# Kernel tuning notes

Measured on AMD Instinct MI355X. Metric: run time of the kernel, lower is better.

## Reference

```python
import jax, jax.numpy as jnp
import numpy as np

B, S, D, H = 4, 4096, 1024, 16
DV = D // H


def setup_inputs() -> dict:
    key = jax.random.key(0)
    ks = jax.random.split(key, 8)
    def gl(k, shape):  # glorot-uniform-ish init
        fan_in, fan_out = shape[0], shape[-1]
        lim = np.sqrt(6.0 / (fan_in + fan_out)).astype(np.float32)
        return jax.random.uniform(k, shape, jnp.float32, -lim, lim)
    return {
        "q": jax.random.normal(ks[0], (B, S, D), jnp.float32),
        "k": jax.random.normal(ks[1], (B, S, D), jnp.float32),
        "v": jax.random.normal(ks[2], (B, S, D), jnp.float32),
        "wq": gl(ks[3], (D, H)), "bq": jnp.zeros((H,), jnp.float32),
        "wk": gl(ks[4], (D, H)), "bk": jnp.zeros((H,), jnp.float32),
        "wv": gl(ks[5], (D, D)), "bv": jnp.zeros((D,), jnp.float32),
        "wo": gl(ks[6], (D, D)), "bo": jnp.zeros((D,), jnp.float32),
    }


def reference(q, k, v, wq, bq, wk, bk, wv, bv, wo, bo):
    b, s, d = q.shape
    h = wq.shape[1]
    dv = d // h
    # per-head scalar queries/keys, sigmoid feature map phi
    qh = jax.nn.sigmoid(q @ wq + bq)                 # (B,S,H)
    kh = jax.nn.sigmoid(k @ wk + bk)                 # (B,S,H)
    vh = (v @ wv + bv).reshape(b, s, h, dv)          # (B,S,H,DV)
    # phi(k)^T @ v contracts seq -> per-head summary (B,H,DV)
    kv = jnp.einsum("bsh,bshd->bhd", kh, vh)
    # NOTE: original tf code cumsums over axis=1 of (B,H,1,DV): the HEAD axis
    state = jnp.cumsum(kv, axis=1)                   # (B,H,DV)
    # phi(q) @ state, broadcast over seq
    out_h = jnp.einsum("bsh,bhd->bshd", qh, state)   # (B,S,H,DV)
    concat = out_h.reshape(b, s, d)
    return concat @ wo + bo                          # (B,S,D)
```

## Files before the change

kernel.cpp:

```cpp
#include <hip/hip_runtime.h>

#define SS 4096
#define DD 1024
#define HH 16

typedef float nfloat4 __attribute__((ext_vector_type(4)));
typedef __attribute__((ext_vector_type(8))) short bf16x8;
typedef __attribute__((ext_vector_type(4))) float f32x4;

__device__ __forceinline__ short f2bf(float f) {
  union { float f; unsigned u; } z; z.f = f;
  return (short)((z.u + 0x8000u) >> 16);
}

__global__ __launch_bounds__(256) void k_wfrag(
    const float* __restrict__ wq, const float* __restrict__ wk,
    short* __restrict__ wf)
{
  const int m = blockIdx.x;
  const float* __restrict__ w = m ? wk : wq;
  short* __restrict__ dst = wf + m * 16384;
  for (int p = threadIdx.x; p < 2048; p += 256) {
    const int t = p >> 6, l = p & 63;
    const int kbase = t*32 + ((l >> 4) * 8), col = l & 15;
    short v[8];
#pragma unroll
    for (int e = 0; e < 8; ++e)
      v[e] = f2bf(w[(size_t)(kbase + e)*HH + col]);
    short* o = dst + (size_t)p * 8;
#pragma unroll
    for (int e = 0; e < 8; ++e) o[e] = v[e];
  }
}

__global__ __launch_bounds__(256, 4) void k_kh(
    const float* __restrict__ k, const short* __restrict__ wf,
    const float* __restrict__ bk, float* __restrict__ kh,
    float* __restrict__ ksp)
{
  const int t = threadIdx.x;
  const int wid = t >> 6, lane = t & 63;
  const int s0 = blockIdx.x * 16;
  const short* __restrict__ wfm = wf + 16384;

  __shared__ short xs[16 * 1024];
  __shared__ float red[1024];

  float4 f[16];
  {
    const float* srow = k + (size_t)s0 * DD + t*4;
#pragma unroll
    for (int j = 0; j < 16; ++j)
      f[j] = *(const float4*)(srow + (size_t)j * DD);
  }
  const short* __restrict__ wfw = wfm + (size_t)(wid*8*64 + lane) * 8;
  bf16x8 afrag[8];
#pragma unroll
  for (int tt = 0; tt < 8; ++tt)
    afrag[tt] = *(const bf16x8*)(wfw + (size_t)(tt*64) * 8);
  __builtin_amdgcn_sched_barrier(0);

#pragma unroll
  for (int j = 0; j < 16; ++j) {
    short4 b4;
    b4.x = f2bf(f[j].x); b4.y = f2bf(f[j].y);
    b4.z = f2bf(f[j].z); b4.w = f2bf(f[j].w);
    const int colb = (t*8) ^ ((j & 7) << 4);
    *(short4*)((char*)xs + j*2048 + colb) = b4;
  }
  __syncthreads();

  const int row = lane & 15, g = lane >> 4;
  const char* __restrict__ xrow = (const char*)xs + row*2048;
  f32x4 acc = {0.f, 0.f, 0.f, 0.f};
#pragma unroll
  for (int tt = 0; tt < 8; ++tt) {
    const int colb = ((wid*256 + tt*32 + g*8) * 2) ^ ((row & 7) << 4);
    const bf16x8 bb = *(const bf16x8*)(xrow + colb);
    acc = __builtin_amdgcn_mfma_f32_16x16x32_bf16(afrag[tt], bb, acc, 0, 0, 0);
  }
  *(f32x4*)&red[(wid*64 + lane)*4] = acc;
  __syncthreads();
  const int orow = t >> 4, ohead = t & 15;
  const int lane2 = ((ohead >> 2) << 4) + orow;
  const int j = ohead & 3;
  const float sacc = red[0*256 + lane2*4 + j] + red[1*256 + lane2*4 + j]
                   + red[2*256 + lane2*4 + j] + red[3*256 + lane2*4 + j];
  const float sig = 1.f/(1.f + __expf(-(sacc + bk[ohead])));
  kh[(size_t)(s0 + orow)*HH + ohead] = sig;
  __syncthreads();
  red[t] = sig;
  __syncthreads();
  if (t < 16) {
    float s = 0.f;
#pragma unroll
    for (int r = 0; r < 16; ++r) s += red[r*16 + t];
    ksp[blockIdx.x*16 + t] = s;
  }
}

__global__ __launch_bounds__(256, 8) void k_kvt(
    const float* __restrict__ v, const float* __restrict__ kh,
    float* __restrict__ part)
{
  const int schunk = blockIdx.x;
  const int dchunk = blockIdx.y;
  const int b = blockIdx.z;
  const int t = threadIdx.x;
  const int c = t & 31;
  const int hh2 = (t >> 5) & 1;
  const int g = t >> 6;
  const int d0 = dchunk*128 + c*4;
  float acc[8][4];
#pragma unroll
  for (int h = 0; h < 8; ++h) {
    acc[h][0] = 0.f; acc[h][1] = 0.f; acc[h][2] = 0.f; acc[h][3] = 0.f;
  }
#pragma unroll 2
  for (int jj = 0; jj < 32; ++jj) {
    const int s = (jj*4 + g)*32 + schunk;
    const size_t rb = (size_t)(b*SS + s);
    const float4 v4 = *(const float4*)(v + rb*DD + d0);
    const float4* khp = (const float4*)(kh + rb*HH) + hh2*2;
    const float4 k0 = khp[0], k1 = khp[1];
    const float kk[8] = {k0.x,k0.y,k0.z,k0.w, k1.x,k1.y,k1.z,k1.w};
#pragma unroll
    for (int h = 0; h < 8; ++h) {
      acc[h][0] = fmaf(kk[h], v4.x, acc[h][0]);
      acc[h][1] = fmaf(kk[h], v4.y, acc[h][1]);
      acc[h][2] = fmaf(kk[h], v4.z, acc[h][2]);
      acc[h][3] = fmaf(kk[h], v4.w, acc[h][3]);
    }
  }
  __shared__ float lds[4][2][128];
  const size_t pbase = (size_t)((b*8 + dchunk)*32 + schunk) * 2048;
#pragma unroll
  for (int h = 0; h < 8; ++h) {
    *(float4*)&lds[g][hh2][c*4] =
        make_float4(acc[h][0], acc[h][1], acc[h][2], acc[h][3]);
    __syncthreads();
    {
      const int hh2r = t >> 7, dl = t & 127;
      const float sum = lds[0][hh2r][dl] + lds[1][hh2r][dl]
                      + lds[2][hh2r][dl] + lds[3][hh2r][dl];
      part[pbase + (hh2r*8 + h)*128 + dl] = sum;
    }
    __syncthreads();
  }
}

__global__ __launch_bounds__(256, 8) void k_red(
    const float* __restrict__ part, float* __restrict__ kvt)
{
  const int dchunk = blockIdx.x;
  const int b = blockIdx.y;
  const int hq = blockIdx.z;
  const int t = threadIdx.x;
  const size_t pb = (size_t)((b*8 + dchunk)*32) * 2048;
#pragma unroll
  for (int ho = 0; ho < 2; ++ho) {
    const int h = hq*4 + ho*2 + (t >> 7), dl = t & 127;
    float s = 0.f;
#pragma unroll 8
    for (int sc = 0; sc < 32; ++sc)
      s += part[pb + (size_t)sc*2048 + h*128 + dl];
    kvt[(size_t)(b*16 + h)*1024 + dchunk*128 + dl] = s;
  }
}

__global__ __launch_bounds__(256, 4) void k_kv(
    const float* __restrict__ kvt, const float* __restrict__ wv,
    float* __restrict__ kvp)
{
  const int h = blockIdx.x;
  const int b = blockIdx.y;
  const int dq = blockIdx.z;
  const int t = threadIdx.x;
  const int w = t >> 6, lane = t & 63;
  __shared__ float kvs[256];
  __shared__ float red[256];
  kvs[t] = kvt[(size_t)(b*16 + h)*1024 + dq*256 + t];
  __syncthreads();
  const float* __restrict__ wp = wv + (size_t)(dq*256 + w*64)*DD + h*64 + lane;
  float acc = 0.f;
#pragma unroll 16
  for (int i = 0; i < 64; ++i)
    acc = fmaf(kvs[w*64 + i], wp[(size_t)i*DD], acc);
  red[t] = acc;
  __syncthreads();
  if (t < 64)
    kvp[((size_t)(b*16 + h)*4 + dq)*64 + t] =
        red[t] + red[64+t] + red[128+t] + red[192+t];
}

__global__ __launch_bounds__(256) void k_kvfin(
    const float* __restrict__ kvp, const float* __restrict__ ksp,
    const float* __restrict__ bv, float* __restrict__ kv)
{
  const int b = blockIdx.x;
  const int t = threadIdx.x;
  __shared__ float red[256];
  __shared__ float ksum[16];
  float s = 0.f;
#pragma unroll
  for (int m = 0; m < 16; ++m)
    s += ksp[b*4096 + m*256 + t];
  red[t] = s;
  __syncthreads();
  if (t < 16) {
    float ks = 0.f;
#pragma unroll
    for (int g = 0; g < 16; ++g) ks += red[g*16 + t];
    ksum[t] = ks;
  }
  __syncthreads();
#pragma unroll
  for (int j = 0; j < 4; ++j) {
    const int idx = j*256 + t;
    const int h = idx >> 6;
    const float* kp = kvp + (size_t)(b*16 + h)*256 + (idx & 63);
    kv[(size_t)b*1024 + idx] =
        kp[0] + kp[64] + kp[128] + kp[192] + ksum[h]*bv[idx];
  }
}

__global__ __launch_bounds__(256) void k_w2(
    const float* __restrict__ kv, const float* __restrict__ wo,
    float* __restrict__ W2)
{
  const int bh = blockIdx.x;
  const int b = bh >> 4, h = bh & 15;
  const int t = threadIdx.x;
  __shared__ float st[64];
  if (t < 64) {
    float s = 0.f;
    for (int hp = 0; hp <= h; ++hp) s += kv[(size_t)b*1024 + hp*64 + t];
    st[t] = s;
  }
  __syncthreads();
  const int d0 = t * 4;
  float4 acc = {0.f, 0.f, 0.f, 0.f};
#pragma unroll 4
  for (int dv = 0; dv < 64; ++dv) {
    const float sv = st[dv];
    const float4 w4 = *(const float4*)(wo + (size_t)(h*64 + dv)*DD + d0);
    acc.x = fmaf(sv, w4.x, acc.x);
    acc.y = fmaf(sv, w4.y, acc.y);
    acc.z = fmaf(sv, w4.z, acc.z);
    acc.w = fmaf(sv, w4.w, acc.w);
  }
  *(float4*)(W2 + (size_t)(b*HH + h)*DD + d0) = acc;
}

__global__ __launch_bounds__(256, 4) void k_qout(
    const float* __restrict__ q, const short* __restrict__ wf,
    const float* __restrict__ bq, const float* __restrict__ W2,
    const float* __restrict__ bo, float* __restrict__ out)
{
  const int t = threadIdx.x;
  const int wid = t >> 6, lane = t & 63;
  const int tile = blockIdx.x;
  const int b = tile >> 8;
  const int s0 = tile * 16;

  __shared__ short xs[16 * 1024];
  __shared__ float red[1024];
  __shared__ float qs[256];

  float4 f[16];
  {
    const float* srow = q + (size_t)s0 * DD + t*4;
#pragma unroll
    for (int j = 0; j < 16; ++j)
      f[j] = *(const float4*)(srow + (size_t)j * DD);
  }
  const short* __restrict__ wfw = wf + (size_t)(wid*8*64 + lane) * 8;
  bf16x8 afrag[8];
#pragma unroll
  for (int tt = 0; tt < 8; ++tt)
    afrag[tt] = *(const bf16x8*)(wfw + (size_t)(tt*64) * 8);
  __builtin_amdgcn_sched_barrier(0);

#pragma unroll
  for (int j = 0; j < 16; ++j) {
    short4 b4;
    b4.x = f2bf(f[j].x); b4.y = f2bf(f[j].y);
    b4.z = f2bf(f[j].z); b4.w = f2bf(f[j].w);
    const int colb = (t*8) ^ ((j & 7) << 4);
    *(short4*)((char*)xs + j*2048 + colb) = b4;
  }
  __syncthreads();

  const int row = lane & 15, g = lane >> 4;
  const char* __restrict__ xrow = (const char*)xs + row*2048;
  f32x4 acc = {0.f, 0.f, 0.f, 0.f};
#pragma unroll
  for (int tt = 0; tt < 8; ++tt) {
    const int colb = ((wid*256 + tt*32 + g*8) * 2) ^ ((row & 7) << 4);
    const bf16x8 bb = *(const bf16x8*)(xrow + colb);
    acc = __builtin_amdgcn_mfma_f32_16x16x32_bf16(afrag[tt], bb, acc, 0, 0, 0);
  }
  *(f32x4*)&red[(wid*64 + lane)*4] = acc;
  __syncthreads();
  {
    const int orow = t >> 4, ohead = t & 15;
    const int lane2 = ((ohead >> 2) << 4) + orow;
    const int j = ohead & 3;
    const float sacc = red[0*256 + lane2*4 + j] + red[1*256 + lane2*4 + j]
                     + red[2*256 + lane2*4 + j] + red[3*256 + lane2*4 + j];
    const float val = sacc + bq[ohead];
    qs[orow*16 + ohead] = 1.f/(1.f + __expf(-val));
  }
  __syncthreads();

  float4 w2[16];
  {
    const float* w2p = W2 + (size_t)(b*HH)*DD + t*4;
#pragma unroll
    for (int h = 0; h < 16; ++h) w2[h] = *(const float4*)(w2p + h*DD);
  }
  const float4 bo4 = *(const float4*)(bo + t*4);

#pragma unroll
  for (int r = 0; r < 16; ++r) {
    float4 o = bo4;
#pragma unroll
    for (int h = 0; h < 16; ++h) {
      const float qv = qs[r*16 + h];
      o.x = fmaf(qv, w2[h].x, o.x);
      o.y = fmaf(qv, w2[h].y, o.y);
      o.z = fmaf(qv, w2[h].z, o.z);
      o.w = fmaf(qv, w2[h].w, o.w);
    }
    nfloat4 ov = { o.x, o.y, o.z, o.w };
    nfloat4* dst = (nfloat4*)(out + (size_t)(s0 + r)*DD + t*4);
    __builtin_nontemporal_store(ov, dst);
  }
}

extern "C" void kernel_launch(void* const* d_in, const int* in_sizes, int n_in,
                              void* d_out, int out_size, void* d_ws, size_t ws_size,
                              hipStream_t stream)
{
  const float* q  = (const float*)d_in[0];
  const float* k  = (const float*)d_in[1];
  const float* v  = (const float*)d_in[2];
  const float* wq = (const float*)d_in[3];
  const float* bq = (const float*)d_in[4];
  const float* wk = (const float*)d_in[5];
  const float* bk = (const float*)d_in[6];
  const float* wv = (const float*)d_in[7];
  const float* bv = (const float*)d_in[8];
  const float* wo = (const float*)d_in[9];
  const float* bo = (const float*)d_in[10];
  float* out = (float*)d_out;
  float* ws  = (float*)d_ws;

  float* kh  = ws;
  float* kvt = ws + 262144;
  float* kvp = ws + 327680;
  float* ksp = ws + 344064;
  float* kv  = ws + 360448;
  float* W2  = ws + 364544;
  short* wf  = (short*)(ws + 430080);
  float* part = out;

  hipLaunchKernelGGL(k_wfrag, dim3(2), dim3(256), 0, stream,
                     wq, wk, wf);
  hipLaunchKernelGGL(k_kh, dim3(1024), dim3(256), 0, stream,
                     k, wf, bk, kh, ksp);
  hipLaunchKernelGGL(k_kvt, dim3(32, 8, 4), dim3(256), 0, stream,
                     v, kh, part);
  hipLaunchKernelGGL(k_red, dim3(8, 4, 4), dim3(256), 0, stream,
                     part, kvt);
  hipLaunchKernelGGL(k_kv, dim3(16, 4, 4), dim3(256), 0, stream,
                     kvt, wv, kvp);
  hipLaunchKernelGGL(k_kvfin, dim3(4), dim3(256), 0, stream,
                     kvp, ksp, bv, kv);
  hipLaunchKernelGGL(k_w2, dim3(64), dim3(256), 0, stream,
                     kv, wo, W2);
  hipLaunchKernelGGL(k_qout, dim3(1024), dim3(256), 0, stream,
                     q, wf, bq, W2, bo, out);
}
```

Measured before the change: 79.13 us.

## Process two row tiles per block in k_kh and k_qout with prefetch of next tile

Each block of k_kh and k_qout now handles two 16-row tiles instead of one, halving the grid. The weight fragments and W2/bias loads are amortized over both tiles, and the second tile's input rows are loaded into registers while the first tile is converted and multiplied. The aim is to hide global load latency and cut per-block setup. The cost is more registers per thread (launch bounds lowered to 2 blocks per SM) and fewer blocks to spread across CUs.

```diff
diff --git a/kernel.cpp b/kernel.cpp
--- a/kernel.cpp
+++ b/kernel.cpp
@@ -33,69 +33,83 @@
   }
 }
 
-__global__ __launch_bounds__(256, 4) void k_kh(
+__global__ __launch_bounds__(256, 2) void k_kh(
     const float* __restrict__ k, const short* __restrict__ wf,
     const float* __restrict__ bk, float* __restrict__ kh,
     float* __restrict__ ksp)
 {
   const int t = threadIdx.x;
   const int wid = t >> 6, lane = t & 63;
-  const int s0 = blockIdx.x * 16;
+  const int tb = blockIdx.x * 2;
   const short* __restrict__ wfm = wf + 16384;
 
   __shared__ short xs[16 * 1024];
   __shared__ float red[1024];
 
+  const short* __restrict__ wfw = wfm + (size_t)(wid*8*64 + lane) * 8;
+  bf16x8 afrag[8];
+#pragma unroll
+  for (int tt = 0; tt < 8; ++tt)
+    afrag[tt] = *(const bf16x8*)(wfw + (size_t)(tt*64) * 8);
+
   float4 f[16];
   {
-    const float* srow = k + (size_t)s0 * DD + t*4;
+    const float* srow = k + (size_t)(tb*16) * DD + t*4;
 #pragma unroll
     for (int j = 0; j < 16; ++j)
       f[j] = *(const float4*)(srow + (size_t)j * DD);
   }
-  const short* __restrict__ wfw = wfm + (size_t)(wid*8*64 + lane) * 8;
-  bf16x8 afrag[8];
-#pragma unroll
-  for (int tt = 0; tt < 8; ++tt)
-    afrag[tt] = *(const bf16x8*)(wfw + (size_t)(tt*64) * 8);
   __builtin_amdgcn_sched_barrier(0);
 
-#pragma unroll
-  for (int j = 0; j < 16; ++j) {
-    short4 b4;
-    b4.x = f2bf(f[j].x); b4.y = f2bf(f[j].y);
-    b4.z = f2bf(f[j].z); b4.w = f2bf(f[j].w);
-    const int colb = (t*8) ^ ((j & 7) << 4);
-    *(short4*)((char*)xs + j*2048 + colb) = b4;
-  }
-  __syncthreads();
-
   const int row = lane & 15, g = lane >> 4;
-  const char* __restrict__ xrow = (const char*)xs + row*2048;
-  f32x4 acc = {0.f, 0.f, 0.f, 0.f};
-#pragma unroll
-  for (int tt = 0; tt < 8; ++tt) {
-    const int colb = ((wid*256 + tt*32 + g*8) * 2) ^ ((row & 7) << 4);
-    const bf16x8 bb = *(const bf16x8*)(xrow + colb);
-    acc = __builtin_amdgcn_mfma_f32_16x16x32_bf16(afrag[tt], bb, acc, 0, 0, 0);
-  }
-  *(f32x4*)&red[(wid*64 + lane)*4] = acc;
-  __syncthreads();
   const int orow = t >> 4, ohead = t & 15;
   const int lane2 = ((ohead >> 2) << 4) + orow;
-  const int j = ohead & 3;
-  const float sacc = red[0*256 + lane2*4 + j] + red[1*256 + lane2*4 + j]
-                   + red[2*256 + lane2*4 + j] + red[3*256 + lane2*4 + j];
-  const float sig = 1.f/(1.f + __expf(-(sacc + bk[ohead])));
-  kh[(size_t)(s0 + orow)*HH + ohead] = sig;
-  __syncthreads();
-  red[t] = sig;
-  __syncthreads();
-  if (t < 16) {
-    float s = 0.f;
-#pragma unroll
-    for (int r = 0; r < 16; ++r) s += red[r*16 + t];
-    ksp[blockIdx.x*16 + t] = s;
+  const int jr = ohead & 3;
+  const float biasv = bk[ohead];
+
+#pragma unroll
+  for (int i = 0; i < 2; ++i) {
+    const int s0 = (tb + i) * 16;
+#pragma unroll
+    for (int j = 0; j < 16; ++j) {
+      short4 b4;
+      b4.x = f2bf(f[j].x); b4.y = f2bf(f[j].y);
+      b4.z = f2bf(f[j].z); b4.w = f2bf(f[j].w);
+      const int colb = (t*8) ^ ((j & 7) << 4);
+      *(short4*)((char*)xs + j*2048 + colb) = b4;
+    }
+    if (i == 0) {
+      const float* srow = k + (size_t)((tb + 1)*16) * DD + t*4;
+#pragma unroll
+      for (int j = 0; j < 16; ++j)
+        f[j] = *(const float4*)(srow + (size_t)j * DD);
+      __builtin_amdgcn_sched_barrier(0);
+    }
+    __syncthreads();
+
+    const char* __restrict__ xrow = (const char*)xs + row*2048;
+    f32x4 acc = {0.f, 0.f, 0.f, 0.f};
+#pragma unroll
+    for (int tt = 0; tt < 8; ++tt) {
+      const int colb = ((wid*256 + tt*32 + g*8) * 2) ^ ((row & 7) << 4);
+      const bf16x8 bb = *(const bf16x8*)(xrow + colb);
+      acc = __builtin_amdgcn_mfma_f32_16x16x32_bf16(afrag[tt], bb, acc, 0, 0, 0);
+    }
+    *(f32x4*)&red[(wid*64 + lane)*4] = acc;
+    __syncthreads();
+    const float sacc = red[0*256 + lane2*4 + jr] + red[1*256 + lane2*4 + jr]
+                     + red[2*256 + lane2*4 + jr] + red[3*256 + lane2*4 + jr];
+    const float sig = 1.f/(1.f + __expf(-(sacc + biasv)));
+    kh[(size_t)(s0 + orow)*HH + ohead] = sig;
+    __syncthreads();
+    red[t] = sig;
+    __syncthreads();
+    if (t < 16) {
+      float s = 0.f;
+#pragma unroll
+      for (int r = 0; r < 16; ++r) s += red[r*16 + t];
+      ksp[(tb + i)*16 + t] = s;
+    }
   }
 }
 
@@ -252,67 +266,24 @@
   *(float4*)(W2 + (size_t)(b*HH + h)*DD + d0) = acc;
 }
 
-__global__ __launch_bounds__(256, 4) void k_qout(
+__global__ __launch_bounds__(256, 2) void k_qout(
     const float* __restrict__ q, const short* __restrict__ wf,
     const float* __restrict__ bq, const float* __restrict__ W2,
     const float* __restrict__ bo, float* __restrict__ out)
 {
   const int t = threadIdx.x;
   const int wid = t >> 6, lane = t & 63;
-  const int tile = blockIdx.x;
-  const int b = tile >> 8;
-  const int s0 = tile * 16;
-
+  const int tb = blockIdx.x * 2;
+  const int b = tb >> 8;
   __shared__ short xs[16 * 1024];
   __shared__ float red[1024];
   __shared__ float qs[256];
 
-  float4 f[16];
-  {
-    const float* srow = q + (size_t)s0 * DD + t*4;
-#pragma unroll
-    for (int j = 0; j < 16; ++j)
-      f[j] = *(const float4*)(srow + (size_t)j * DD);
-  }
   const short* __restrict__ wfw = wf + (size_t)(wid*8*64 + lane) * 8;
   bf16x8 afrag[8];
 #pragma unroll
   for (int tt = 0; tt < 8; ++tt)
     afrag[tt] = *(const bf16x8*)(wfw + (size_t)(tt*64) * 8);
-  __builtin_amdgcn_sched_barrier(0);
-
-#pragma unroll
-  for (int j = 0; j < 16; ++j) {
-    short4 b4;
-    b4.x = f2bf(f[j].x); b4.y = f2bf(f[j].y);
-    b4.z = f2bf(f[j].z); b4.w = f2bf(f[j].w);
-    const int colb = (t*8) ^ ((j & 7) << 4);
-    *(short4*)((char*)xs + j*2048 + colb) = b4;
-  }
-  __syncthreads();
-
-  const int row = lane & 15, g = lane >> 4;
-  const char* __restrict__ xrow = (const char*)xs + row*2048;
-  f32x4 acc = {0.f, 0.f, 0.f, 0.f};
-#pragma unroll
-  for (int tt = 0; tt < 8; ++tt) {
-    const int colb = ((wid*256 + tt*32 + g*8) * 2) ^ ((row & 7) << 4);
-    const bf16x8 bb = *(const bf16x8*)(xrow + colb);
-    acc = __builtin_amdgcn_mfma_f32_16x16x32_bf16(afrag[tt], bb, acc, 0, 0, 0);
-  }
-  *(f32x4*)&red[(wid*64 + lane)*4] = acc;
-  __syncthreads();
-  {
-    const int orow = t >> 4, ohead = t & 15;
-    const int lane2 = ((ohead >> 2) << 4) + orow;
-    const int j = ohead & 3;
-    const float sacc = red[0*256 + lane2*4 + j] + red[1*256 + lane2*4 + j]
-                     + red[2*256 + lane2*4 + j] + red[3*256 + lane2*4 + j];
-    const float val = sacc + bq[ohead];
-    qs[orow*16 + ohead] = 1.f/(1.f + __expf(-val));
-  }
-  __syncthreads();
-
   float4 w2[16];
   {
     const float* w2p = W2 + (size_t)(b*HH)*DD + t*4;
@@ -321,20 +292,74 @@
   }
   const float4 bo4 = *(const float4*)(bo + t*4);
 
-#pragma unroll
-  for (int r = 0; r < 16; ++r) {
-    float4 o = bo4;
-#pragma unroll
-    for (int h = 0; h < 16; ++h) {
-      const float qv = qs[r*16 + h];
-      o.x = fmaf(qv, w2[h].x, o.x);
-      o.y = fmaf(qv, w2[h].y, o.y);
-      o.z = fmaf(qv, w2[h].z, o.z);
-      o.w = fmaf(qv, w2[h].w, o.w);
-    }
-    nfloat4 ov = { o.x, o.y, o.z, o.w };
-    nfloat4* dst = (nfloat4*)(out + (size_t)(s0 + r)*DD + t*4);
-    __builtin_nontemporal_store(ov, dst);
+  float4 f[16];
+  {
+    const float* srow = q + (size_t)(tb*16) * DD + t*4;
+#pragma unroll
+    for (int j = 0; j < 16; ++j)
+      f[j] = *(const float4*)(srow + (size_t)j * DD);
+  }
+  __builtin_amdgcn_sched_barrier(0);
+
+  const int row = lane & 15, g = lane >> 4;
+  const int orow = t >> 4, ohead = t & 15;
+  const int lane2 = ((ohead >> 2) << 4) + orow;
+  const int jr = ohead & 3;
+  const float biasv = bq[ohead];
+
+#pragma unroll
+  for (int i = 0; i < 2; ++i) {
+    const int s0 = (tb + i) * 16;
+#pragma unroll
+    for (int j = 0; j < 16; ++j) {
+      short4 b4;
+      b4.x = f2bf(f[j].x); b4.y = f2bf(f[j].y);
+      b4.z = f2bf(f[j].z); b4.w = f2bf(f[j].w);
+      const int colb = (t*8) ^ ((j & 7) << 4);
+      *(short4*)((char*)xs + j*2048 + colb) = b4;
+    }
+    if (i == 0) {
+      const float* srow = q + (size_t)((tb + 1)*16) * DD + t*4;
+#pragma unroll
+      for (int j = 0; j < 16; ++j)
+        f[j] = *(const float4*)(srow + (size_t)j * DD);
+      __builtin_amdgcn_sched_barrier(0);
+    }
+    __syncthreads();
+
+    const char* __restrict__ xrow = (const char*)xs + row*2048;
+    f32x4 acc = {0.f, 0.f, 0.f, 0.f};
+#pragma unroll
+    for (int tt = 0; tt < 8; ++tt) {
+      const int colb = ((wid*256 + tt*32 + g*8) * 2) ^ ((row & 7) << 4);
+      const bf16x8 bb = *(const bf16x8*)(xrow + colb);
+      acc = __builtin_amdgcn_mfma_f32_16x16x32_bf16(afrag[tt], bb, acc, 0, 0, 0);
+    }
+    *(f32x4*)&red[(wid*64 + lane)*4] = acc;
+    __syncthreads();
+    {
+      const float sacc = red[0*256 + lane2*4 + jr] + red[1*256 + lane2*4 + jr]
+                       + red[2*256 + lane2*4 + jr] + red[3*256 + lane2*4 + jr];
+      const float val = sacc + biasv;
+      qs[t] = 1.f/(1.f + __expf(-val));
+    }
+    __syncthreads();
+
+#pragma unroll
+    for (int r = 0; r < 16; ++r) {
+      float4 o = bo4;
+#pragma unroll
+      for (int h = 0; h < 16; ++h) {
+        const float qv = qs[r*16 + h];
+        o.x = fmaf(qv, w2[h].x, o.x);
+        o.y = fmaf(qv, w2[h].y, o.y);
+        o.z = fmaf(qv, w2[h].z, o.z);
+        o.w = fmaf(qv, w2[h].w, o.w);
+      }
+      nfloat4 ov = { o.x, o.y, o.z, o.w };
+      nfloat4* dst = (nfloat4*)(out + (size_t)(s0 + r)*DD + t*4);
+      __builtin_nontemporal_store(ov, dst);
+    }
   }
 }
 
@@ -367,7 +392,7 @@
 
   hipLaunchKernelGGL(k_wfrag, dim3(2), dim3(256), 0, stream,
                      wq, wk, wf);
-  hipLaunchKernelGGL(k_kh, dim3(1024), dim3(256), 0, stream,
+  hipLaunchKernelGGL(k_kh, dim3(512), dim3(256), 0, stream,
                      k, wf, bk, kh, ksp);
   hipLaunchKernelGGL(k_kvt, dim3(32, 8, 4), dim3(256), 0, stream,
                      v, kh, part);
@@ -379,6 +404,6 @@
                      kvp, ksp, bv, kv);
   hipLaunchKernelGGL(k_w2, dim3(64), dim3(256), 0, stream,
                      kv, wo, W2);
-  hipLaunchKernelGGL(k_qout, dim3(1024), dim3(256), 0, stream,
+  hipLaunchKernelGGL(k_qout, dim3(512), dim3(256), 0, stream,
                      q, wf, bq, W2, bo, out);
 }
```

Measured after the change: 81.48 us. +3.0%, slower.
